# Optimization experiments

Measured on AMD Instinct MI355X. Metric: run time of the kernel, lower is better.

## Reference

```python
import jax, jax.numpy as jnp
import numpy as np

B, N, NFEAT = 8, 2048, 128
RED = NFEAT // 2          # 64
K_G = 8                   # hard-coded ksize in LUMLP -> DSgroupMLP
K_LU = 16                 # k for FeatureLaplacian
EPS = 1e-5                # BatchNorm eps (torch default)


def _bn_relu(y, g, b):
    # BatchNorm1d in training mode: biased batch stats over (batch, spatial)
    mu = y.mean(axis=(0, 2), keepdims=True)
    var = y.var(axis=(0, 2), keepdims=True)
    return jax.nn.relu((y - mu) * jax.lax.rsqrt(var + EPS) * g[None, :, None] + b[None, :, None])


def _cbr(x, W, b, g, bt):
    # ConvBNReLU1D with kernel_size=1: pointwise linear + BN + ReLU
    y = jnp.einsum('oc,bcn->bon', W, x) + b[None, :, None]
    return _bn_relu(y, g, bt)


def _bknn(x, k):
    # x: [B, C, N]; returns top-k nearest-neighbor indices [B, N, k]
    inner = 2.0 * jnp.einsum('bcn,bcm->bnm', x, x)
    xx = jnp.sum(x * x, axis=1)                         # [B, N]
    dist = xx[:, :, None] - inner + xx[:, None, :]      # [B, N, N]
    return jax.lax.top_k(-dist, k)[1]


def setup_inputs() -> dict:
    key = jax.random.key(0)
    ks = jax.random.split(key, 8)
    def w(k_, o, i):
        return jax.random.normal(k_, (o, i), jnp.float32) / np.sqrt(i)
    return {
        'xyz': jax.random.normal(ks[0], (B, 3, N), jnp.float32),
        'feat': jax.random.normal(ks[1], (B, NFEAT, N), jnp.float32),
        # mlp1: nfeat -> redfeat
        'w1': w(ks[2], RED, NFEAT), 'b1': jnp.zeros((RED,), jnp.float32),
        'g1': jnp.ones((RED,), jnp.float32), 'be1': jnp.zeros((RED,), jnp.float32),
        # DSgroupMLP fc1 + bn1
        'wf': w(ks[3], RED, RED), 'bf': jnp.zeros((RED,), jnp.float32),
        'gg': jnp.ones((RED,), jnp.float32), 'bg': jnp.zeros((RED,), jnp.float32),
        # FeatureLaplacian transform + batchNorm
        'wl': w(ks[4], RED, RED), 'bl': jnp.zeros((RED,), jnp.float32),
        'gl': jnp.ones((RED,), jnp.float32), 'bel': jnp.zeros((RED,), jnp.float32),
        # mlp2: redfeat -> nfeat
        'w2': w(ks[5], NFEAT, RED), 'b2': jnp.zeros((NFEAT,), jnp.float32),
        'g2': jnp.ones((NFEAT,), jnp.float32), 'be2': jnp.zeros((NFEAT,), jnp.float32),
        # mlp3: nfeat -> 2*nfeat
        'w3': w(ks[6], 2 * NFEAT, NFEAT), 'b3': jnp.zeros((2 * NFEAT,), jnp.float32),
        'g3': jnp.ones((2 * NFEAT,), jnp.float32), 'be3': jnp.zeros((2 * NFEAT,), jnp.float32),
    }


def reference(xyz, feat, w1, b1, g1, be1, wf, bf, gg, bg, wl, bl, gl, bel,
              w2, b2, g2, be2, w3, b3, g3, be3):
    # ---- mlp1 ----
    x = _cbr(feat, w1, b1, g1, be1)                      # [B, RED, N]
    Bm, Fm, Nm = x.shape
    # ---- DSgroupMLP (ksize = 8) ----
    idx = _bknn(xyz[:, :2, :], K_G)                      # [B, N, K]
    def gather_g(fb, ib):
        # faithful torch .view: [F, N*K] -> [F, K, N]
        return fb[:, ib.reshape(-1)].reshape(Fm, K_G, Nm)
    grp = jax.vmap(gather_g)(x, idx)                     # [B, F, K, N]
    gq = grp.transpose(0, 3, 2, 1)                       # [B, N, K, F]
    h = jnp.einsum('bnkf,of->bnko', gq, wf) + bf         # fc1 over F
    h = h.reshape(Bm, Nm * K_G, Fm).transpose(0, 2, 1)   # [B, F, N*K]
    h = _bn_relu(h, gg, bg)
    x = h.reshape(Bm, Fm, Nm, K_G).max(axis=-1)          # max-pool over K
    # ---- FeatureLaplacian (k = 16) ----
    idx2 = _bknn(xyz[:, :2, :], K_LU)                    # [B, N, k]
    def lapfn(fb, ib):
        # faithful torch .view: [F, N*k] -> [N, k, F]
        lf = fb[:, ib.reshape(-1)].reshape(Nm, K_LU, Fm)
        return fb.T - lf.mean(axis=1)                    # [N, F]
    lap = jax.vmap(lapfn)(x, idx2)                       # [B, N, F]
    t = jnp.einsum('bnf,of->bon', lap, wl) + bl[None, :, None]  # [B, F, N]
    t = _bn_relu(t, gl, bel)
    x = x + t
    # ---- mlp2 + residual + mlp3 ----
    y = _cbr(x, w2, b2, g2, be2) + feat                  # [B, NFEAT, N]
    return _cbr(y, w3, b3, g3, be3)                      # [B, 2*NFEAT, N]
```

## Files before the change

### kernel.cpp

```cpp
#include <hip/hip_runtime.h>

#define NB   8
#define NPT  2048
#define NF   128
#define CR   64
#define EPSI 1e-5

__global__ void __launch_bounds__(256) knn_kernel(const float* __restrict__ xyz,
                                                  int* __restrict__ idx16) {
  __shared__ float px[NPT], py[NPT], sxx[NPT];
  int b = blockIdx.x >> 9;
  const float* xb = xyz + b * 3 * NPT;
  for (int i = threadIdx.x; i < NPT; i += 256) {
    float x = xb[i], y = xb[NPT + i];
    px[i] = x; py[i] = y;
    sxx[i] = __fadd_rn(__fmul_rn(x, x), __fmul_rn(y, y));
  }
  __syncthreads();
  int lane = threadIdx.x & 63, wid = threadIdx.x >> 6;
  int q = ((blockIdx.x & 511) << 2) | wid;
  float qx = px[q], qy = py[q], qxx = sxx[q];
  float dc[32];
#pragma unroll 4
  for (int j = 0; j < 32; ++j) {
    int m = lane + (j << 6);
    float inner_s = __fmaf_rn(qy, py[m], __fmul_rn(qx, px[m]));
    dc[j] = __fadd_rn(__fsub_rn(qxx, __fmul_rn(2.0f, inner_s)), sxx[m]);
  }
  int keep = 0;
  for (int r = 0; r < 16; ++r) {
    float dmin = dc[0]; int jmin = 0;
#pragma unroll
    for (int j = 1; j < 32; ++j) {
      bool better = dc[j] < dmin;
      dmin = better ? dc[j] : dmin;
      jmin = better ? j : jmin;
    }
    float hd = dmin;
    int   hm = lane + (jmin << 6);
#pragma unroll
    for (int off = 1; off < 64; off <<= 1) {
      float od = __shfl_xor(hd, off);
      int   om = __shfl_xor(hm, off);
      bool take = (od < hd) || (od == hd && om < hm);
      hd = take ? od : hd;
      hm = take ? om : hm;
    }
    if (lane == r) keep = hm;
    bool own = (hm & 63) == lane;
    int jw = hm >> 6;
#pragma unroll
    for (int j = 0; j < 32; ++j)
      dc[j] = (own && j == jw) ? 1e38f : dc[j];
  }
  if (lane < 16) idx16[((b * NPT + q) << 4) + lane] = keep;
}

template<int IC, int OC>
__global__ void __launch_bounds__(256) conv_stats(const float* __restrict__ in,
                                                  const float* __restrict__ w,
                                                  const float* __restrict__ bias,
                                                  float* __restrict__ outp,
                                                  double* __restrict__ stats) {
  int bz = blockIdx.x;
  int n  = ((bz & 7) << 8) | threadIdx.x;
  int o0 = ((bz >> 3) % (OC / 8)) * 8;
  int b  = bz / (8 * (OC / 8));
  const float* inb = in + b * IC * NPT + n;
  float a[8];
#pragma unroll
  for (int t = 0; t < 8; ++t) a[t] = bias[o0 + t];
  const float* wb = w + o0 * IC;
#pragma unroll 4
  for (int f = 0; f < IC; ++f) {
    float v = inb[f * NPT];
#pragma unroll
    for (int t = 0; t < 8; ++t) a[t] += wb[t * IC + f] * v;
  }
  float* ob = outp + b * OC * NPT + n;
#pragma unroll
  for (int t = 0; t < 8; ++t) ob[(o0 + t) * NPT] = a[t];
  __shared__ double red[4][8][2];
  int lane = threadIdx.x & 63, wid = threadIdx.x >> 6;
#pragma unroll
  for (int j = 0; j < 8; ++j) {
    double s1 = (double)a[j];
    double s2 = (double)a[j] * (double)a[j];
#pragma unroll
    for (int off = 32; off; off >>= 1) { s1 += __shfl_down(s1, off); s2 += __shfl_down(s2, off); }
    if (lane == 0) { red[wid][j][0] = s1; red[wid][j][1] = s2; }
  }
  __syncthreads();
  if (threadIdx.x < 8) {
    int j = threadIdx.x;
    double S1 = red[0][j][0] + red[1][j][0] + red[2][j][0] + red[3][j][0];
    double S2 = red[0][j][1] + red[1][j][1] + red[2][j][1] + red[3][j][1];
    atomicAdd(&stats[o0 + j], S1);
    atomicAdd(&stats[OC + o0 + j], S2);
  }
}

template<int IC, int OC>
__global__ void __launch_bounds__(256) conv_stats16(const float* __restrict__ in,
                                                    const float* __restrict__ w,
                                                    const float* __restrict__ bias,
                                                    float* __restrict__ outp,
                                                    double* __restrict__ stats) {
  int bz = blockIdx.x;
  int n  = ((bz & 7) << 8) | threadIdx.x;
  int o0 = ((bz >> 3) % (OC / 16)) * 16;
  int b  = bz / (8 * (OC / 16));
  const float* inb = in + b * IC * NPT + n;
  float a[16];
#pragma unroll
  for (int t = 0; t < 16; ++t) a[t] = bias[o0 + t];
  const float* wb = w + o0 * IC;
#pragma unroll 2
  for (int f = 0; f < IC; ++f) {
    float v = inb[f * NPT];
#pragma unroll
    for (int t = 0; t < 16; ++t) a[t] += wb[t * IC + f] * v;
  }
  float* ob = outp + b * OC * NPT + n;
#pragma unroll
  for (int t = 0; t < 16; ++t) ob[(o0 + t) * NPT] = a[t];
  __shared__ double red[4][16][2];
  int lane = threadIdx.x & 63, wid = threadIdx.x >> 6;
#pragma unroll
  for (int j = 0; j < 16; ++j) {
    double s1 = (double)a[j];
    double s2 = (double)a[j] * (double)a[j];
#pragma unroll
    for (int off = 32; off; off >>= 1) { s1 += __shfl_down(s1, off); s2 += __shfl_down(s2, off); }
    if (lane == 0) { red[wid][j][0] = s1; red[wid][j][1] = s2; }
  }
  __syncthreads();
  if (threadIdx.x < 16) {
    int j = threadIdx.x;
    double S1 = red[0][j][0] + red[1][j][0] + red[2][j][0] + red[3][j][0];
    double S2 = red[0][j][1] + red[1][j][1] + red[2][j][1] + red[3][j][1];
    atomicAdd(&stats[o0 + j], S1);
    atomicAdd(&stats[OC + o0 + j], S2);
  }
}

template<int C>
__global__ void __launch_bounds__(256) bn_apply(const float* __restrict__ pre,
                                                const float* __restrict__ addsrc,
                                                float* __restrict__ outp,
                                                const double* __restrict__ stats,
                                                const float* __restrict__ gam,
                                                const float* __restrict__ bet,
                                                double inv_cnt) {
  __shared__ float sc[C], sh[C];
  for (int c = threadIdx.x; c < C; c += 256) {
    double mu    = stats[c] * inv_cnt;
    double var   = stats[C + c] * inv_cnt - mu * mu;
    double scale = (double)gam[c] / sqrt(var + EPSI);
    sc[c] = (float)scale;
    sh[c] = (float)((double)bet[c] - mu * scale);
  }
  __syncthreads();
  const float4* pre4 = (const float4*)pre;
  const float4* add4 = (const float4*)addsrc;
  float4* out4 = (float4*)outp;
  int total4 = NB * C * (NPT / 4);
  for (int i = blockIdx.x * 256 + threadIdx.x; i < total4; i += gridDim.x * 256) {
    int c = (i >> 9) & (C - 1);
    float s = sc[c], h = sh[c];
    float4 v = pre4[i];
    v.x = fmaxf(v.x * s + h, 0.f);
    v.y = fmaxf(v.y * s + h, 0.f);
    v.z = fmaxf(v.z * s + h, 0.f);
    v.w = fmaxf(v.w * s + h, 0.f);
    if (addsrc) {
      float4 a = add4[i];
      v.x += a.x; v.y += a.y; v.z += a.z; v.w += a.w;
    }
    out4[i] = v;
  }
}

__global__ void __launch_bounds__(256) dsgroup_kernel(const float* __restrict__ x1,
                                                      const int* __restrict__ idx16,
                                                      const float* __restrict__ wf,
                                                      const float* __restrict__ bfp,
                                                      float* __restrict__ hmax,
                                                      double* __restrict__ stats) {
  __shared__ float wfT[64 * 65];
  __shared__ double dred[4][64][2];
  for (int i = threadIdx.x; i < 64 * 64; i += 256) {
    int o = i >> 6, f = i & 63;
    wfT[f * 65 + o] = wf[i];
  }
  __syncthreads();
  int lane = threadIdx.x & 63, wid = threadIdx.x >> 6;
  int wave = blockIdx.x * 4 + wid;
  float bo = bfp[lane];
  double s1 = 0.0, s2 = 0.0;
  for (int p = 0; p < 4; ++p) {
    int pt = wave * 4 + p;
    int b = pt >> 11, n = pt & 2047;
    int src[8];
#pragma unroll
    for (int k = 0; k < 8; ++k) {
      int j = k * NPT + n;
      src[k] = __builtin_amdgcn_readfirstlane(idx16[((b * NPT + (j >> 3)) << 4) | (j & 7)]);
    }
    float acc[8];
#pragma unroll
    for (int k = 0; k < 8; ++k) acc[k] = bo;
    const float* x1b = x1 + b * CR * NPT;
    for (int f = 0; f < 64; ++f) {
      float wv = wfT[f * 65 + lane];
      const float* row = x1b + f * NPT;
#pragma unroll
      for (int k = 0; k < 8; ++k) acc[k] += row[src[k]] * wv;
    }
    float hm = acc[0];
#pragma unroll
    for (int k = 0; k < 8; ++k) {
      hm = fmaxf(hm, acc[k]);
      s1 += (double)acc[k];
      s2 += (double)acc[k] * (double)acc[k];
    }
    hmax[(b * CR + lane) * NPT + n] = hm;
  }
  dred[wid][lane][0] = s1; dred[wid][lane][1] = s2;
  __syncthreads();
  if (threadIdx.x < 64) {
    double S1 = dred[0][threadIdx.x][0] + dred[1][threadIdx.x][0] + dred[2][threadIdx.x][0] + dred[3][threadIdx.x][0];
    double S2 = dred[0][threadIdx.x][1] + dred[1][threadIdx.x][1] + dred[2][threadIdx.x][1] + dred[3][threadIdx.x][1];
    atomicAdd(&stats[threadIdx.x], S1);
    atomicAdd(&stats[64 + threadIdx.x], S2);
  }
}

__global__ void __launch_bounds__(256) lap_fused(const float* __restrict__ hpre,
                                                 const int* __restrict__ idx16,
                                                 const float* __restrict__ wl,
                                                 const float* __restrict__ blp,
                                                 float* __restrict__ tpre,
                                                 double* __restrict__ stats,
                                                 const double* __restrict__ stg,
                                                 const float* __restrict__ gg,
                                                 const float* __restrict__ bg) {
  __shared__ float wlT[64 * 65];
  __shared__ double dred[4][64][2];
  __shared__ float vstage[4][64];
  __shared__ float scg[64], shg[64];
  for (int i = threadIdx.x; i < 64 * 64; i += 256) {
    int o = i >> 6, f = i & 63;
    wlT[f * 65 + o] = wl[i];
  }
  if (threadIdx.x < 64) {
    int c = threadIdx.x;
    double mu  = stg[c] / 131072.0;
    double var = stg[64 + c] / 131072.0 - mu * mu;
    double s   = (double)gg[c] / sqrt(var + EPSI);
    scg[c] = (float)s;
    shg[c] = (float)((double)bg[c] - mu * s);
  }
  __syncthreads();
  int lane = threadIdx.x & 63, wid = threadIdx.x >> 6;
  int g = lane >> 4, cc = lane & 15;
  float blv = blp[lane];
  double s1 = 0.0, s2 = 0.0;
  for (int p = 0; p < 4; ++p) {
    int pt = (blockIdx.x * 4 + wid) * 4 + p;
    int b = pt >> 11, n = pt & 2047;
    int ch = n >> 5;
    int r0 = (n & 31) << 6;
    const float* xrow = hpre + (b * CR + ch) * NPT;
    const int* ib = idx16 + ((b * NPT + r0) << 4);
    float sgc = scg[ch], shc = shg[ch];
    float msum = 0.f;
#pragma unroll
    for (int kk = 0; kk < 16; ++kk) {
      int sidx = ib[(((kk << 2) + g) << 4) | cc];
      msum += fmaxf(fmaf(xrow[sidx], sgc, shc), 0.f);
    }
    float mval = msum * 0.0625f;
    float xraw = hpre[(b * CR + lane) * NPT + n];
    float xv = fmaxf(fmaf(xraw, scg[lane], shg[lane]), 0.f);
    vstage[wid][lane] = xv - mval;
    float acc = blv;
    for (int f = 0; f < 64; ++f)
      acc += wlT[f * 65 + lane] * vstage[wid][f];
    tpre[(b * CR + lane) * NPT + n] = acc;
    s1 += (double)acc;
    s2 += (double)acc * (double)acc;
  }
  dred[wid][lane][0] = s1; dred[wid][lane][1] = s2;
  __syncthreads();
  if (threadIdx.x < 64) {
    double S1 = dred[0][threadIdx.x][0] + dred[1][threadIdx.x][0] + dred[2][threadIdx.x][0] + dred[3][threadIdx.x][0];
    double S2 = dred[0][threadIdx.x][1] + dred[1][threadIdx.x][1] + dred[2][threadIdx.x][1] + dred[3][threadIdx.x][1];
    atomicAdd(&stats[threadIdx.x], S1);
    atomicAdd(&stats[64 + threadIdx.x], S2);
  }
}

__global__ void __launch_bounds__(256) conv2_fused(const float* __restrict__ hpre,
                                                   const float* __restrict__ tpre,
                                                   const double* __restrict__ stg,
                                                   const float* __restrict__ gg,
                                                   const float* __restrict__ bg,
                                                   const double* __restrict__ stl,
                                                   const float* __restrict__ gl,
                                                   const float* __restrict__ bel,
                                                   const float* __restrict__ w,
                                                   const float* __restrict__ bias,
                                                   float* __restrict__ outp,
                                                   double* __restrict__ stats) {
  __shared__ float scg[64], shg[64], scl[64], shl[64];
  __shared__ double red[4][8][2];
  if (threadIdx.x < 64) {
    int c = threadIdx.x;
    double mu  = stg[c] / 131072.0;
    double var = stg[64 + c] / 131072.0 - mu * mu;
    double s   = (double)gg[c] / sqrt(var + EPSI);
    scg[c] = (float)s; shg[c] = (float)((double)bg[c] - mu * s);
    double mu2  = stl[c] / 16384.0;
    double var2 = stl[64 + c] / 16384.0 - mu2 * mu2;
    double s2   = (double)gl[c] / sqrt(var2 + EPSI);
    scl[c] = (float)s2; shl[c] = (float)((double)bel[c] - mu2 * s2);
  }
  __syncthreads();
  int bz = blockIdx.x;
  int n  = ((bz & 7) << 8) | threadIdx.x;
  int o0 = ((bz >> 3) % 16) * 8;
  int b  = bz / 128;
  const float* hb = hpre + b * CR * NPT + n;
  const float* tb = tpre + b * CR * NPT + n;
  float a[8];
#pragma unroll
  for (int t = 0; t < 8; ++t) a[t] = bias[o0 + t];
  const float* wb = w + o0 * CR;
#pragma unroll 4
  for (int f = 0; f < CR; ++f) {
    float hv = hb[f * NPT], tv = tb[f * NPT];
    float v = fmaxf(fmaf(hv, scg[f], shg[f]), 0.f) + fmaxf(fmaf(tv, scl[f], shl[f]), 0.f);
#pragma unroll
    for (int t = 0; t < 8; ++t) a[t] += wb[t * CR + f] * v;
  }
  float* ob = outp + b * NF * NPT + n;
#pragma unroll
  for (int t = 0; t < 8; ++t) ob[(o0 + t) * NPT] = a[t];
  int lane = threadIdx.x & 63, wid = threadIdx.x >> 6;
#pragma unroll
  for (int j = 0; j < 8; ++j) {
    double s1 = (double)a[j];
    double s2 = (double)a[j] * (double)a[j];
#pragma unroll
    for (int off = 32; off; off >>= 1) { s1 += __shfl_down(s1, off); s2 += __shfl_down(s2, off); }
    if (lane == 0) { red[wid][j][0] = s1; red[wid][j][1] = s2; }
  }
  __syncthreads();
  if (threadIdx.x < 8) {
    int j = threadIdx.x;
    double S1 = red[0][j][0] + red[1][j][0] + red[2][j][0] + red[3][j][0];
    double S2 = red[0][j][1] + red[1][j][1] + red[2][j][1] + red[3][j][1];
    atomicAdd(&stats[o0 + j], S1);
    atomicAdd(&stats[NF + o0 + j], S2);
  }
}

extern "C" void kernel_launch(void* const* d_in, const int* in_sizes, int n_in,
                              void* d_out, int out_size, void* d_ws, size_t ws_size,
                              hipStream_t stream) {
  const float* xyz  = (const float*)d_in[0];
  const float* feat = (const float*)d_in[1];
  const float* w1   = (const float*)d_in[2];
  const float* b1   = (const float*)d_in[3];
  const float* g1   = (const float*)d_in[4];
  const float* be1  = (const float*)d_in[5];
  const float* wf   = (const float*)d_in[6];
  const float* bf   = (const float*)d_in[7];
  const float* gg   = (const float*)d_in[8];
  const float* bg   = (const float*)d_in[9];
  const float* wl   = (const float*)d_in[10];
  const float* bl   = (const float*)d_in[11];
  const float* gl   = (const float*)d_in[12];
  const float* bel  = (const float*)d_in[13];
  const float* w2   = (const float*)d_in[14];
  const float* b2   = (const float*)d_in[15];
  const float* g2   = (const float*)d_in[16];
  const float* be2  = (const float*)d_in[17];
  const float* w3   = (const float*)d_in[18];
  const float* b3   = (const float*)d_in[19];
  const float* g3   = (const float*)d_in[20];
  const float* be3  = (const float*)d_in[21];
  float* out = (float*)d_out;

  float* x1   = out;
  float* tpre = out + 1048576;
  int*  idx16 = (int*)(out + 2097152);
  float*  hpre  = (float*)d_ws;
  float*  y2    = hpre + 1048576;
  double* stats = (double*)((char*)d_ws + (12u << 20));
  double* st0 = stats;
  double* stg = stats + 128;
  double* stl = stats + 256;
  double* st2 = stats + 384;
  double* st3 = stats + 640;

  hipMemsetAsync(stats, 0, 1152 * sizeof(double), stream);

  knn_kernel<<<4096, 256, 0, stream>>>(xyz, idx16);
  conv_stats<128, 64><<<512, 256, 0, stream>>>(feat, w1, b1, x1, st0);
  bn_apply<64><<<1024, 256, 0, stream>>>(x1, nullptr, x1, st0, g1, be1, 1.0 / 16384.0);
  dsgroup_kernel<<<1024, 256, 0, stream>>>(x1, idx16, wf, bf, hpre, stg);
  lap_fused<<<1024, 256, 0, stream>>>(hpre, idx16, wl, bl, tpre, stl, stg, gg, bg);
  conv2_fused<<<1024, 256, 0, stream>>>(hpre, tpre, stg, gg, bg, stl, gl, bel, w2, b2, y2, st2);
  bn_apply<128><<<1024, 256, 0, stream>>>(y2, feat, y2, st2, g2, be2, 1.0 / 16384.0);
  conv_stats16<128, 256><<<1024, 256, 0, stream>>>(y2, w3, b3, out, st3);
  bn_apply<256><<<1024, 256, 0, stream>>>(out, nullptr, out, st3, g3, be3, 1.0 / 16384.0);
}
```

Measured before the change: 306.2 us.

## Apply fc1 before neighbor gather and fuse BN1 into the pointwise conv

Since fc1 is linear, the 64x64 projection is computed once per point into a point-major buffer, and the grouping step then only gathers 8 precomputed rows and takes max and stats. This replaces the per-neighbor 64-wide matmul on gathered data (8x redundant FLOPs with scattered reads). The mlp1 BatchNorm+ReLU is folded into the new conv's input load, which removes a separate bn_apply pass. The mlp3 conv now uses the 8-output-channel template with twice the blocks instead of the 16-channel variant. The new point-major z buffer lives in the output region after idx16, which is a workspace-aliasing risk.

Measured after the change: 257.0 us. 1.19x faster.

```diff
diff --git a/kernel.cpp b/kernel.cpp
--- a/kernel.cpp
+++ b/kernel.cpp
@@ -92,50 +92,6 @@
   }
   __syncthreads();
   if (threadIdx.x < 8) {
-    int j = threadIdx.x;
-    double S1 = red[0][j][0] + red[1][j][0] + red[2][j][0] + red[3][j][0];
-    double S2 = red[0][j][1] + red[1][j][1] + red[2][j][1] + red[3][j][1];
-    atomicAdd(&stats[o0 + j], S1);
-    atomicAdd(&stats[OC + o0 + j], S2);
-  }
-}
-
-template<int IC, int OC>
-__global__ void __launch_bounds__(256) conv_stats16(const float* __restrict__ in,
-                                                    const float* __restrict__ w,
-                                                    const float* __restrict__ bias,
-                                                    float* __restrict__ outp,
-                                                    double* __restrict__ stats) {
-  int bz = blockIdx.x;
-  int n  = ((bz & 7) << 8) | threadIdx.x;
-  int o0 = ((bz >> 3) % (OC / 16)) * 16;
-  int b  = bz / (8 * (OC / 16));
-  const float* inb = in + b * IC * NPT + n;
-  float a[16];
-#pragma unroll
-  for (int t = 0; t < 16; ++t) a[t] = bias[o0 + t];
-  const float* wb = w + o0 * IC;
-#pragma unroll 2
-  for (int f = 0; f < IC; ++f) {
-    float v = inb[f * NPT];
-#pragma unroll
-    for (int t = 0; t < 16; ++t) a[t] += wb[t * IC + f] * v;
-  }
-  float* ob = outp + b * OC * NPT + n;
-#pragma unroll
-  for (int t = 0; t < 16; ++t) ob[(o0 + t) * NPT] = a[t];
-  __shared__ double red[4][16][2];
-  int lane = threadIdx.x & 63, wid = threadIdx.x >> 6;
-#pragma unroll
-  for (int j = 0; j < 16; ++j) {
-    double s1 = (double)a[j];
-    double s2 = (double)a[j] * (double)a[j];
-#pragma unroll
-    for (int off = 32; off; off >>= 1) { s1 += __shfl_down(s1, off); s2 += __shfl_down(s2, off); }
-    if (lane == 0) { red[wid][j][0] = s1; red[wid][j][1] = s2; }
-  }
-  __syncthreads();
-  if (threadIdx.x < 16) {
     int j = threadIdx.x;
     double S1 = red[0][j][0] + red[1][j][0] + red[2][j][0] + red[3][j][0];
     double S2 = red[0][j][1] + red[1][j][1] + red[2][j][1] + red[3][j][1];
@@ -181,48 +137,68 @@
   }
 }
 
-__global__ void __launch_bounds__(256) dsgroup_kernel(const float* __restrict__ x1,
-                                                      const int* __restrict__ idx16,
-                                                      const float* __restrict__ wf,
-                                                      const float* __restrict__ bfp,
-                                                      float* __restrict__ hmax,
-                                                      double* __restrict__ stats) {
-  __shared__ float wfT[64 * 65];
+__global__ void __launch_bounds__(256) zconv_kernel(const float* __restrict__ x1pre,
+                                                    const double* __restrict__ st0,
+                                                    const float* __restrict__ g1,
+                                                    const float* __restrict__ be1,
+                                                    const float* __restrict__ wf,
+                                                    const float* __restrict__ bfp,
+                                                    float* __restrict__ zT) {
+  __shared__ float sc[64], sh[64];
+  if (threadIdx.x < 64) {
+    int c = threadIdx.x;
+    double mu  = st0[c] / 16384.0;
+    double var = st0[64 + c] / 16384.0 - mu * mu;
+    double s   = (double)g1[c] / sqrt(var + EPSI);
+    sc[c] = (float)s;
+    sh[c] = (float)((double)be1[c] - mu * s);
+  }
+  __syncthreads();
+  int bz = blockIdx.x;
+  int n  = ((bz & 7) << 8) | threadIdx.x;
+  int o0 = ((bz >> 3) % 8) * 8;
+  int b  = bz / 64;
+  const float* inb = x1pre + b * CR * NPT + n;
+  float a[8];
+#pragma unroll
+  for (int t = 0; t < 8; ++t) a[t] = bfp[o0 + t];
+  const float* wb = wf + o0 * CR;
+#pragma unroll 4
+  for (int f = 0; f < CR; ++f) {
+    float v = fmaxf(fmaf(inb[f * NPT], sc[f], sh[f]), 0.f);
+#pragma unroll
+    for (int t = 0; t < 8; ++t) a[t] += wb[t * CR + f] * v;
+  }
+  float* zp = zT + ((b * NPT + n) << 6) + o0;
+  *(float4*)(zp)     = make_float4(a[0], a[1], a[2], a[3]);
+  *(float4*)(zp + 4) = make_float4(a[4], a[5], a[6], a[7]);
+}
+
+__global__ void __launch_bounds__(256) gathermax_kernel(const float* __restrict__ zT,
+                                                        const int* __restrict__ idx16,
+                                                        float* __restrict__ hmax,
+                                                        double* __restrict__ stats) {
   __shared__ double dred[4][64][2];
-  for (int i = threadIdx.x; i < 64 * 64; i += 256) {
-    int o = i >> 6, f = i & 63;
-    wfT[f * 65 + o] = wf[i];
-  }
-  __syncthreads();
   int lane = threadIdx.x & 63, wid = threadIdx.x >> 6;
   int wave = blockIdx.x * 4 + wid;
-  float bo = bfp[lane];
   double s1 = 0.0, s2 = 0.0;
   for (int p = 0; p < 4; ++p) {
     int pt = wave * 4 + p;
     int b = pt >> 11, n = pt & 2047;
-    int src[8];
+    const float* zb = zT + ((b * NPT) << 6);
+    float vals[8];
 #pragma unroll
     for (int k = 0; k < 8; ++k) {
       int j = k * NPT + n;
-      src[k] = __builtin_amdgcn_readfirstlane(idx16[((b * NPT + (j >> 3)) << 4) | (j & 7)]);
-    }
-    float acc[8];
-#pragma unroll
-    for (int k = 0; k < 8; ++k) acc[k] = bo;
-    const float* x1b = x1 + b * CR * NPT;
-    for (int f = 0; f < 64; ++f) {
-      float wv = wfT[f * 65 + lane];
-      const float* row = x1b + f * NPT;
-#pragma unroll
-      for (int k = 0; k < 8; ++k) acc[k] += row[src[k]] * wv;
-    }
-    float hm = acc[0];
+      int src = idx16[((b * NPT + (j >> 3)) << 4) | (j & 7)];
+      vals[k] = zb[(src << 6) + lane];
+    }
+    float hm = vals[0];
 #pragma unroll
     for (int k = 0; k < 8; ++k) {
-      hm = fmaxf(hm, acc[k]);
-      s1 += (double)acc[k];
-      s2 += (double)acc[k] * (double)acc[k];
+      hm = fmaxf(hm, vals[k]);
+      s1 += (double)vals[k];
+      s2 += (double)vals[k] * (double)vals[k];
     }
     hmax[(b * CR + lane) * NPT + n] = hm;
   }
@@ -393,9 +369,10 @@
   const float* be3  = (const float*)d_in[21];
   float* out = (float*)d_out;
 
-  float* x1   = out;
-  float* tpre = out + 1048576;
-  int*  idx16 = (int*)(out + 2097152);
+  float* x1pre = out;
+  float* tpre  = out + 1048576;
+  int*  idx16  = (int*)(out + 2097152);
+  float* zT    = out + 2359296;
   float*  hpre  = (float*)d_ws;
   float*  y2    = hpre + 1048576;
   double* stats = (double*)((char*)d_ws + (12u << 20));
@@ -408,12 +385,12 @@
   hipMemsetAsync(stats, 0, 1152 * sizeof(double), stream);
 
   knn_kernel<<<4096, 256, 0, stream>>>(xyz, idx16);
-  conv_stats<128, 64><<<512, 256, 0, stream>>>(feat, w1, b1, x1, st0);
-  bn_apply<64><<<1024, 256, 0, stream>>>(x1, nullptr, x1, st0, g1, be1, 1.0 / 16384.0);
-  dsgroup_kernel<<<1024, 256, 0, stream>>>(x1, idx16, wf, bf, hpre, stg);
+  conv_stats<128, 64><<<512, 256, 0, stream>>>(feat, w1, b1, x1pre, st0);
+  zconv_kernel<<<512, 256, 0, stream>>>(x1pre, st0, g1, be1, wf, bf, zT);
+  gathermax_kernel<<<1024, 256, 0, stream>>>(zT, idx16, hpre, stg);
   lap_fused<<<1024, 256, 0, stream>>>(hpre, idx16, wl, bl, tpre, stl, stg, gg, bg);
   conv2_fused<<<1024, 256, 0, stream>>>(hpre, tpre, stg, gg, bg, stl, gl, bel, w2, b2, y2, st2);
   bn_apply<128><<<1024, 256, 0, stream>>>(y2, feat, y2, st2, g2, be2, 1.0 / 16384.0);
-  conv_stats16<128, 256><<<1024, 256, 0, stream>>>(y2, w3, b3, out, st3);
+  conv_stats<128, 256><<<2048, 256, 0, stream>>>(y2, w3, b3, out, st3);
   bn_apply<256><<<1024, 256, 0, stream>>>(out, nullptr, out, st3, g3, be3, 1.0 / 16384.0);
 }
```
